# Performance work log

Measured on AMD Instinct MI355X. Metric: run time of the kernel, lower is better.

Reference implementation:

```python
import jax, jax.numpy as jnp
import numpy as np

B = 32768          # number of trees
DEPTH = 3          # perfect binary trees: 8 leaves each
N_LEAF = B * (1 << DEPTH)
V, X, H, C = 32000, 256, 128, 5


def _apply_iou(iou, c, b_iou):
    # iou: [n, 3H], c: [n, H]
    i, o, u = jnp.split(iou + b_iou, 3, axis=1)
    c = jax.nn.sigmoid(i) * jnp.tanh(u) + c
    h = jax.nn.sigmoid(o) * jnp.tanh(c)
    return h, c


def setup_inputs() -> dict:
    key = jax.random.key(0)
    ks = jax.random.split(key, 8)
    rng = np.random.default_rng(0)

    # per-level random node orderings -> irregular child gathers
    sizes = [N_LEAF >> l for l in range(DEPTH + 1)]  # [8B, 4B, 2B, B]
    perms = [rng.permutation(s).astype(np.int32) for s in sizes]
    parts = []
    for l in range(1, DEPTH + 1):
        n = sizes[l]
        k = np.arange(n)
        ci = np.empty((n, 2), np.int32)
        # canonical node k at level l has children 2k, 2k+1 at level l-1
        ci[perms[l]] = np.stack([perms[l - 1][2 * k], perms[l - 1][2 * k + 1]], 1)
        parts.append(ci)
    child_idx = jnp.asarray(np.concatenate(parts, 0))  # [4B+2B+B, 2]

    leaf_x = jax.random.randint(ks[0], (N_LEAF,), 0, V, dtype=jnp.int32)
    sc = 0.02
    return {
        "leaf_x": leaf_x,
        "child_idx": child_idx,
        "emb": jax.random.normal(ks[1], (V, X), jnp.float32) * sc,
        "W_iou": jax.random.normal(ks[2], (3 * H, X), jnp.float32) * sc,
        "U_iou": jax.random.normal(ks[3], (3 * H, 2 * H), jnp.float32) * sc,
        "b_iou": jnp.zeros((3 * H,), jnp.float32),
        "U_f": jax.random.normal(ks[4], (2 * H, 2 * H), jnp.float32) * sc,
        "b_f": jnp.zeros((2 * H,), jnp.float32),
        "W_lin": jax.random.normal(ks[5], (C, H), jnp.float32) * sc,
        "b_lin": jnp.zeros((C,), jnp.float32),
    }


def reference(leaf_x, child_idx, emb, W_iou, U_iou, b_iou, U_f, b_f, W_lin, b_lin):
    # Leaves: embedding -> W_iou -> gates with c=0 (dropout is identity in eval)
    embeds = emb[leaf_x]                       # [N_leaf, X]
    iou = embeds @ W_iou.T                     # [N_leaf, 3H]
    h, c = _apply_iou(iou, jnp.zeros((leaf_x.shape[0], H), iou.dtype), b_iou)

    hs = [h]
    n, offset, total = leaf_x.shape[0], 0, child_idx.shape[0]
    while offset < total:  # one iteration per tree level (static)
        n //= 2
        ci = child_idx[offset:offset + n]       # [n, 2] -> prev-level rows
        offset += n
        h_ch = h[ci]                            # [n, 2, H] irregular gather
        c_ch = c[ci]                            # [n, 2, H]
        h_cat = h_ch.reshape(n, 2 * H)
        f = jax.nn.sigmoid(h_cat @ U_f.T + b_f).reshape(n, 2, H)
        c_sum = jnp.sum(f * c_ch, axis=1)       # [n, H]
        iou = h_cat @ U_iou.T                   # [n, 3H]
        h, c = _apply_iou(iou, c_sum, b_iou)
        hs.append(h)

    h_all = jnp.concatenate(hs, axis=0)         # [N_total, H]
    logits = h_all @ W_lin.T + b_lin            # [N_total, C]
    return logits
```

## Files before the change

### kernel.cpp

```cpp
#include <hip/hip_runtime.h>
#include <hip/hip_bf16.h>
#include <stdint.h>


#define THREADS 512

typedef __attribute__((ext_vector_type(8))) short short8;
typedef __attribute__((ext_vector_type(4))) float f32x4;
typedef f32x4 __attribute__((aligned(4))) f32x4u;

__device__ __forceinline__ unsigned short f2bf(float x) {
    unsigned u = __float_as_uint(x);
    u += 0x7fffu + ((u >> 16) & 1u);
    return (unsigned short)(u >> 16);
}
__device__ __forceinline__ float bf2f(unsigned short b) {
    return __uint_as_float(((unsigned)b) << 16);
}
__device__ __forceinline__ float sigm(float x) { return 1.0f / (1.0f + __expf(-x)); }

__global__ __launch_bounds__(256)
void prep_kernel(const float* __restrict__ W_iou,
                 const float* __restrict__ U_iou,
                 const float* __restrict__ U_f,
                 unsigned short* __restrict__ Wl,
                 unsigned short* __restrict__ Wc)
{
    const int i = blockIdx.x * 256 + threadIdx.x;
    if (i < 98304) {
        Wl[i] = f2bf(W_iou[i]);
        Wc[i] = f2bf(U_iou[i]);
    }
    if (i < 65536) {
        Wc[98304 + i] = f2bf(U_f[i]);
    }
}

template<int NCOL, int G, bool WC>
__device__ __forceinline__ void level_step(
    const unsigned short* __restrict__ Wg,
    const unsigned char* Blds,
    unsigned char* h_out,
    unsigned short* c_out,
    const unsigned short* c_prev, int nslot_prev,
    const float* __restrict__ b_iou, const float* __restrict__ b_f,
    int w, int lrow, int lk, int nslot_out, int mvalid)
{
    const int q0 = w * 16;
    const unsigned char* wbase = reinterpret_cast<const unsigned char*>(Wg)
                               + (q0 + lrow) * 512 + lk * 16;

    f32x4 acc[NCOL][G];
    #pragma unroll
    for (int j = 0; j < NCOL; ++j)
        #pragma unroll
        for (int g = 0; g < G; ++g)
            acc[j][g] = (f32x4){0.f, 0.f, 0.f, 0.f};

    short8 a0[NCOL], a1[NCOL];
    #pragma unroll
    for (int j = 0; j < NCOL; ++j)
        a0[j] = *reinterpret_cast<const short8*>(wbase + j * 65536);

    #pragma unroll
    for (int ks = 0; ks < 8; ++ks) {
        if (ks < 7) {
            #pragma unroll
            for (int j = 0; j < NCOL; ++j) {
                short8 v = *reinterpret_cast<const short8*>(
                    wbase + j * 65536 + (ks + 1) * 64);
                if (ks & 1) a0[j] = v; else a1[j] = v;
            }
        }
        #pragma unroll
        for (int g = 0; g < G; ++g) {
            const int row = g * 16 + lrow;
            const int chunk = (ks * 4 + lk) ^ (row & 7);
            short8 bN = *reinterpret_cast<const short8*>(
                Blds + row * 512 + (chunk << 4));
            #pragma unroll
            for (int j = 0; j < NCOL; ++j) {
                short8 a = (ks & 1) ? a1[j] : a0[j];
                acc[j][g] = __builtin_amdgcn_mfma_f32_16x16x32_bf16(
                    a, bN, acc[j][g], 0, 0, 0);
            }
        }
    }

    #pragma unroll
    for (int g = 0; g < G; ++g) {
        const int ml = g * 16 + lrow;
        if (ml < mvalid) {
            #pragma unroll
            for (int r = 0; r < 4; ++r) {
                const int p = q0 + lk * 4 + r;
                float iv = acc[0][g][r] + b_iou[p];
                float ov = acc[1][g][r] + b_iou[128 + p];
                float uv = acc[2][g][r] + b_iou[256 + p];
                float csum = 0.f;
                if (NCOL == 5) {
                    float f0 = acc[3][g][r] + b_f[p];
                    float f1 = acc[4][g][r] + b_f[128 + p];
                    csum = sigm(f0) * bf2f(c_prev[p * nslot_prev + 2 * ml])
                         + sigm(f1) * bf2f(c_prev[p * nslot_prev + 2 * ml + 1]);
                }
                float cv = sigm(iv) * tanhf(uv) + csum;
                float hv = sigm(ov) * tanhf(cv);
                if (WC) c_out[p * nslot_out + ml] = f2bf(cv);
                const int jr = ml >> 1;
                const int q = (ml & 1) * 16 + (p >> 3);
                *reinterpret_cast<unsigned short*>(
                    h_out + jr * 512 + ((q ^ (jr & 7)) << 4) + (p & 7) * 2)
                    = f2bf(hv);
            }
        }
    }
}

__device__ __forceinline__ void logits_emit(
    const unsigned char* h_lds, int M, const int* idsLds, int idBase,
    int segOff, const float* __restrict__ W_lin, const float* __restrict__ b_lin,
    float* __restrict__ out, int t)
{
    const int s = t >> 2, sub = t & 3;
    if (s >= M) return;
    float hv[32];
    const int j = s >> 1;
    #pragma unroll
    for (int qq = 0; qq < 4; ++qq) {
        const int q = (s & 1) * 16 + sub * 4 + qq;
        short8 v = *reinterpret_cast<const short8*>(
            h_lds + j * 512 + ((q ^ (j & 7)) << 4));
        #pragma unroll
        for (int e = 0; e < 8; ++e) hv[qq * 8 + e] = bf2f((unsigned short)v[e]);
    }
    const int gid = idsLds ? idsLds[s] : (idBase + s);
    float dots[5];
    #pragma unroll
    for (int cl = 0; cl < 5; ++cl) {
        const float* wr = W_lin + cl * 128 + sub * 32;
        float d = 0.f;
        #pragma unroll
        for (int k = 0; k < 32; ++k) d += hv[k] * wr[k];
        d += __shfl_xor(d, 1);
        d += __shfl_xor(d, 2);
        dots[cl] = d;
    }
    if (sub == 0) {
        float* op = out + (size_t)(segOff + gid) * 5;
        f32x4 v4 = { dots[0] + b_lin[0], dots[1] + b_lin[1],
                     dots[2] + b_lin[2], dots[3] + b_lin[3] };
        *reinterpret_cast<f32x4u*>(op) = v4;
        op[4] = dots[4] + b_lin[4];
    }
}

__global__ __launch_bounds__(THREADS, 4)
void tree_kernel(const int*  __restrict__ leaf_x,
                 const int2* __restrict__ cpairs,
                 const float* __restrict__ emb,
                 const unsigned short* __restrict__ Wl,
                 const unsigned short* __restrict__ Wc,
                 const float* __restrict__ b_iou,
                 const float* __restrict__ b_f,
                 const float* __restrict__ W_lin,
                 const float* __restrict__ b_lin,
                 float* __restrict__ out)
{
    __shared__ unsigned char arena[65536];
    __shared__ int ids0[64], ids1[32], ids2[16], tok[64];

    const int t    = threadIdx.x;
    const int lane = t & 63;
    const int w    = t >> 6;
    const int lrow = lane & 15;
    const int lk   = lane >> 4;
    const int blk3 = blockIdx.x * 8;

    if (t < 8)  { int2 p = cpairs[196608 + blk3 + t]; ids2[2*t] = p.x; ids2[2*t+1] = p.y; }
    __syncthreads();
    if (t < 16) { int2 p = cpairs[131072 + ids2[t]];  ids1[2*t] = p.x; ids1[2*t+1] = p.y; }
    __syncthreads();
    if (t < 32) { int2 p = cpairs[ids1[t]];           ids0[2*t] = p.x; ids0[2*t+1] = p.y; }
    __syncthreads();
    if (t < 64) { tok[t] = leaf_x[ids0[t]]; }
    __syncthreads();

    unsigned char*  X0 = arena;
    unsigned char*  h0 = arena + 32768;
    unsigned short* c0 = (unsigned short*)(arena + 49152);
    unsigned char*  h1 = arena;
    unsigned short* c1 = (unsigned short*)(arena + 8192);
    unsigned char*  h2 = arena + 32768;
    unsigned short* c2 = (unsigned short*)(arena + 36864);
    unsigned char*  h3 = arena + 16384;

    {
        const int c  = t & 31;
        const int r0 = t >> 5;
        #pragma unroll
        for (int rr = 0; rr < 4; ++rr) {
            const int r  = r0 + rr * 16;
            const int gi = tok[r];
            const float4* src = reinterpret_cast<const float4*>(
                emb + (size_t)gi * 256 + c * 8);
            float4 a = src[0], b = src[1];
            short8 v;
            v[0]=(short)f2bf(a.x); v[1]=(short)f2bf(a.y);
            v[2]=(short)f2bf(a.z); v[3]=(short)f2bf(a.w);
            v[4]=(short)f2bf(b.x); v[5]=(short)f2bf(b.y);
            v[6]=(short)f2bf(b.z); v[7]=(short)f2bf(b.w);
            *reinterpret_cast<short8*>(X0 + r * 512 + ((c ^ (r & 7)) << 4)) = v;
        }
    }
    __syncthreads();

    level_step<3, 4, true>(Wl, X0, h0, c0, nullptr, 0, b_iou, b_f,
                           w, lrow, lk, 64, 64);
    __syncthreads();

    logits_emit(h0, 64, ids0, 0, 0, W_lin, b_lin, out, t);
    level_step<5, 2, true>(Wc, h0, h1, c1, c0, 64, b_iou, b_f,
                           w, lrow, lk, 32, 32);
    __syncthreads();

    logits_emit(h1, 32, ids1, 0, 262144, W_lin, b_lin, out, t);
    level_step<5, 1, true>(Wc, h1, h2, c2, c1, 32, b_iou, b_f,
                           w, lrow, lk, 16, 16);
    __syncthreads();

    logits_emit(h2, 16, ids2, 0, 393216, W_lin, b_lin, out, t);
    level_step<5, 1, false>(Wc, h2, h3, nullptr, c2, 16, b_iou, b_f,
                            w, lrow, lk, 8, 8);
    __syncthreads();

    logits_emit(h3, 8, nullptr, blk3, 458752, W_lin, b_lin, out, t);
}

extern "C" void kernel_launch(void* const* d_in, const int* in_sizes, int n_in,
                              void* d_out, int out_size, void* d_ws, size_t ws_size,
                              hipStream_t stream)
{
    const int*   leaf_x = (const int*)d_in[0];
    const int*   child  = (const int*)d_in[1];
    const float* emb    = (const float*)d_in[2];
    const float* W_iou  = (const float*)d_in[3];
    const float* U_iou  = (const float*)d_in[4];
    const float* b_iou  = (const float*)d_in[5];
    const float* U_f    = (const float*)d_in[6];
    const float* b_f    = (const float*)d_in[7];
    const float* W_lin  = (const float*)d_in[8];
    const float* b_lin  = (const float*)d_in[9];
    float* out = (float*)d_out;

    char* ws = (char*)d_ws;
    unsigned short* Wl = (unsigned short*)ws;
    unsigned short* Wc = (unsigned short*)(ws + 196608);

    prep_kernel<<<384, 256, 0, stream>>>(W_iou, U_iou, U_f, Wl, Wc);

    tree_kernel<<<4096, THREADS, 0, stream>>>(
        leaf_x, (const int2*)child, emb, Wl, Wc,
        b_iou, b_f, W_lin, b_lin, out);
}
```

Baseline: 808.7 us.

## Shrink LDS arena with halved leaf pass and in-place cell state for higher occupancy

The leaf level is processed in two halves of 32 rows, so the embedding tile needs only 16KB. The cell state now lives in one padded array whose stride doubles each level and is updated in place. Together these cut LDS from 64KB to about 52KB, and launch bounds rise to allow 6 blocks per CU. Logit results are stashed in LDS and written out in one pass at the end, and sigmoid/tanh switch to fast reciprocal and exp forms, which costs some accuracy and may add register pressure under the tighter bound.

```diff
diff --git a/kernel.cpp b/kernel.cpp
--- a/kernel.cpp
+++ b/kernel.cpp
@@ -17,7 +17,12 @@
 __device__ __forceinline__ float bf2f(unsigned short b) {
     return __uint_as_float(((unsigned)b) << 16);
 }
-__device__ __forceinline__ float sigm(float x) { return 1.0f / (1.0f + __expf(-x)); }
+__device__ __forceinline__ float rcp_fast(float x) { return __builtin_amdgcn_rcpf(x); }
+__device__ __forceinline__ float sigm(float x) { return rcp_fast(1.f + __expf(-x)); }
+__device__ __forceinline__ float tanh_fast(float x) {
+    float e = __expf(2.f * x);
+    return (e - 1.f) * rcp_fast(e + 1.f);
+}
 
 __global__ __launch_bounds__(256)
 void prep_kernel(const float* __restrict__ W_iou,
@@ -36,15 +41,14 @@
     }
 }
 
-template<int NCOL, int G, bool WC>
+template<int NCOL, int G, int CW, bool WC>
 __device__ __forceinline__ void level_step(
     const unsigned short* __restrict__ Wg,
     const unsigned char* Blds,
     unsigned char* h_out,
-    unsigned short* c_out,
-    const unsigned short* c_prev, int nslot_prev,
+    unsigned short* cAr,
     const float* __restrict__ b_iou, const float* __restrict__ b_f,
-    int w, int lrow, int lk, int nslot_out, int mvalid)
+    int w, int lrow, int lk, int slotBase, int mrows)
 {
     const int q0 = w * 16;
     const unsigned char* wbase = reinterpret_cast<const unsigned char*>(Wg)
@@ -89,8 +93,9 @@
 
     #pragma unroll
     for (int g = 0; g < G; ++g) {
-        const int ml = g * 16 + lrow;
-        if (ml < mvalid) {
+        const int mlB = g * 16 + lrow;
+        if (mlB < mrows) {
+            const int ml = slotBase + mlB;
             #pragma unroll
             for (int r = 0; r < 4; ++r) {
                 const int p = q0 + lk * 4 + r;
@@ -101,12 +106,13 @@
                 if (NCOL == 5) {
                     float f0 = acc[3][g][r] + b_f[p];
                     float f1 = acc[4][g][r] + b_f[128 + p];
-                    csum = sigm(f0) * bf2f(c_prev[p * nslot_prev + 2 * ml])
-                         + sigm(f1) * bf2f(c_prev[p * nslot_prev + 2 * ml + 1]);
+                    const int cb = p * 68 + CW * mlB;
+                    csum = sigm(f0) * bf2f(cAr[cb])
+                         + sigm(f1) * bf2f(cAr[cb + CW / 2]);
                 }
-                float cv = sigm(iv) * tanhf(uv) + csum;
-                float hv = sigm(ov) * tanhf(cv);
-                if (WC) c_out[p * nslot_out + ml] = f2bf(cv);
+                float cv = sigm(iv) * tanh_fast(uv) + csum;
+                float hv = sigm(ov) * tanh_fast(cv);
+                if (WC) cAr[p * 68 + CW * ml] = f2bf(cv);
                 const int jr = ml >> 1;
                 const int q = (ml & 1) * 16 + (p >> 3);
                 *reinterpret_cast<unsigned short*>(
@@ -117,10 +123,9 @@
     }
 }
 
-__device__ __forceinline__ void logits_emit(
-    const unsigned char* h_lds, int M, const int* idsLds, int idBase,
-    int segOff, const float* __restrict__ W_lin, const float* __restrict__ b_lin,
-    float* __restrict__ out, int t)
+__device__ __forceinline__ void logits_stash(
+    const unsigned char* h_lds, int M, int stBase,
+    const float* __restrict__ W_lin, float* sL, int t)
 {
     const int s = t >> 2, sub = t & 3;
     if (s >= M) return;
@@ -134,7 +139,6 @@
         #pragma unroll
         for (int e = 0; e < 8; ++e) hv[qq * 8 + e] = bf2f((unsigned short)v[e]);
     }
-    const int gid = idsLds ? idsLds[s] : (idBase + s);
     float dots[5];
     #pragma unroll
     for (int cl = 0; cl < 5; ++cl) {
@@ -147,15 +151,13 @@
         dots[cl] = d;
     }
     if (sub == 0) {
-        float* op = out + (size_t)(segOff + gid) * 5;
-        f32x4 v4 = { dots[0] + b_lin[0], dots[1] + b_lin[1],
-                     dots[2] + b_lin[2], dots[3] + b_lin[3] };
-        *reinterpret_cast<f32x4u*>(op) = v4;
-        op[4] = dots[4] + b_lin[4];
-    }
-}
-
-__global__ __launch_bounds__(THREADS, 4)
+        #pragma unroll
+        for (int cl = 0; cl < 5; ++cl)
+            sL[(stBase + s) * 5 + cl] = dots[cl];
+    }
+}
+
+__global__ __launch_bounds__(THREADS, 6)
 void tree_kernel(const int*  __restrict__ leaf_x,
                  const int2* __restrict__ cpairs,
                  const float* __restrict__ emb,
@@ -167,8 +169,8 @@
                  const float* __restrict__ b_lin,
                  float* __restrict__ out)
 {
-    __shared__ unsigned char arena[65536];
-    __shared__ int ids0[64], ids1[32], ids2[16], tok[64];
+    __shared__ __align__(16) unsigned char arena[52576];
+    __shared__ int ids0[64], ids1[32], ids2[16], tok[64], sg[120];
 
     const int t    = threadIdx.x;
     const int lane = t & 63;
@@ -183,58 +185,72 @@
     __syncthreads();
     if (t < 32) { int2 p = cpairs[ids1[t]];           ids0[2*t] = p.x; ids0[2*t+1] = p.y; }
     __syncthreads();
-    if (t < 64) { tok[t] = leaf_x[ids0[t]]; }
-    __syncthreads();
-
-    unsigned char*  X0 = arena;
-    unsigned char*  h0 = arena + 32768;
-    unsigned short* c0 = (unsigned short*)(arena + 49152);
-    unsigned char*  h1 = arena;
-    unsigned short* c1 = (unsigned short*)(arena + 8192);
-    unsigned char*  h2 = arena + 32768;
-    unsigned short* c2 = (unsigned short*)(arena + 36864);
-    unsigned char*  h3 = arena + 16384;
-
-    {
-        const int c  = t & 31;
-        const int r0 = t >> 5;
-        #pragma unroll
-        for (int rr = 0; rr < 4; ++rr) {
-            const int r  = r0 + rr * 16;
-            const int gi = tok[r];
-            const float4* src = reinterpret_cast<const float4*>(
-                emb + (size_t)gi * 256 + c * 8);
-            float4 a = src[0], b = src[1];
-            short8 v;
-            v[0]=(short)f2bf(a.x); v[1]=(short)f2bf(a.y);
-            v[2]=(short)f2bf(a.z); v[3]=(short)f2bf(a.w);
-            v[4]=(short)f2bf(b.x); v[5]=(short)f2bf(b.y);
-            v[6]=(short)f2bf(b.z); v[7]=(short)f2bf(b.w);
-            *reinterpret_cast<short8*>(X0 + r * 512 + ((c ^ (r & 7)) << 4)) = v;
-        }
-    }
-    __syncthreads();
-
-    level_step<3, 4, true>(Wl, X0, h0, c0, nullptr, 0, b_iou, b_f,
-                           w, lrow, lk, 64, 64);
-    __syncthreads();
-
-    logits_emit(h0, 64, ids0, 0, 0, W_lin, b_lin, out, t);
-    level_step<5, 2, true>(Wc, h0, h1, c1, c0, 64, b_iou, b_f,
-                           w, lrow, lk, 32, 32);
-    __syncthreads();
-
-    logits_emit(h1, 32, ids1, 0, 262144, W_lin, b_lin, out, t);
-    level_step<5, 1, true>(Wc, h1, h2, c2, c1, 32, b_iou, b_f,
-                           w, lrow, lk, 16, 16);
-    __syncthreads();
-
-    logits_emit(h2, 16, ids2, 0, 393216, W_lin, b_lin, out, t);
-    level_step<5, 1, false>(Wc, h2, h3, nullptr, c2, 16, b_iou, b_f,
-                            w, lrow, lk, 8, 8);
-    __syncthreads();
-
-    logits_emit(h3, 8, nullptr, blk3, 458752, W_lin, b_lin, out, t);
+    if      (t < 64)  { tok[t] = leaf_x[ids0[t]]; sg[t] = ids0[t]; }
+    else if (t < 96)  { sg[t] = 262144 + ids1[t - 64]; }
+    else if (t < 112) { sg[t] = 393216 + ids2[t - 96]; }
+    else if (t < 120) { sg[t] = 458752 + blk3 + (t - 112); }
+    __syncthreads();
+
+    unsigned char*  X0  = arena;
+    unsigned char*  h0  = arena + 16384;
+    unsigned short* cAr = (unsigned short*)(arena + 32768);
+    float*          sL  = (float*)(arena + 50176);
+    unsigned char*  h1  = arena;
+    unsigned char*  h2  = arena + 16384;
+    unsigned char*  h3  = arena;
+
+    #pragma unroll 1
+    for (int half = 0; half < 2; ++half) {
+        {
+            const int c  = t & 31;
+            const int r0 = t >> 5;
+            #pragma unroll
+            for (int rr = 0; rr < 2; ++rr) {
+                const int r  = r0 + rr * 16;
+                const int gi = tok[half * 32 + r];
+                const float4* src = reinterpret_cast<const float4*>(
+                    emb + (size_t)gi * 256 + c * 8);
+                float4 a = src[0], b = src[1];
+                short8 v;
+                v[0]=(short)f2bf(a.x); v[1]=(short)f2bf(a.y);
+                v[2]=(short)f2bf(a.z); v[3]=(short)f2bf(a.w);
+                v[4]=(short)f2bf(b.x); v[5]=(short)f2bf(b.y);
+                v[6]=(short)f2bf(b.z); v[7]=(short)f2bf(b.w);
+                *reinterpret_cast<short8*>(X0 + r * 512 + ((c ^ (r & 7)) << 4)) = v;
+            }
+        }
+        __syncthreads();
+        level_step<3, 2, 1, true>(Wl, X0, h0, cAr, b_iou, b_f,
+                                  w, lrow, lk, half * 32, 32);
+        __syncthreads();
+    }
+
+    logits_stash(h0, 64, 0, W_lin, sL, t);
+    level_step<5, 2, 2, true>(Wc, h0, h1, cAr, b_iou, b_f,
+                              w, lrow, lk, 0, 32);
+    __syncthreads();
+
+    logits_stash(h1, 32, 64, W_lin, sL, t);
+    level_step<5, 1, 4, true>(Wc, h1, h2, cAr, b_iou, b_f,
+                              w, lrow, lk, 0, 16);
+    __syncthreads();
+
+    logits_stash(h2, 16, 96, W_lin, sL, t);
+    level_step<5, 1, 8, false>(Wc, h2, h3, cAr, b_iou, b_f,
+                               w, lrow, lk, 0, 8);
+    __syncthreads();
+
+    logits_stash(h3, 8, 112, W_lin, sL, t);
+    __syncthreads();
+
+    if (t < 120) {
+        const float* sp = sL + t * 5;
+        float* op = out + (size_t)sg[t] * 5;
+        f32x4 v4 = { sp[0] + b_lin[0], sp[1] + b_lin[1],
+                     sp[2] + b_lin[2], sp[3] + b_lin[3] };
+        *reinterpret_cast<f32x4u*>(op) = v4;
+        op[4] = sp[4] + b_lin[4];
+    }
 }
 
 extern "C" void kernel_launch(void* const* d_in, const int* in_sizes, int n_in,
```

Result: slower. 1.210 ms (+49.6%).
